# Performance work log

Measured on AMD Instinct MI355X. Metric: run time of the kernel, lower is better.

The kernel has to match this reference:

```python
import jax, jax.numpy as jnp
import numpy as np

N_USERS = 100000
N_ITEMS = 50000
N = N_USERS + N_ITEMS  # graph nodes
E = 2_400_000
B = 16384
EMB = 64
HID = 128
LN_EPS = 1e-5


def _gcn(x, W, b, src, dst):
    # PyG GCNConv (eval): sym-normalized aggregation with self-loops.
    xw = x @ W                                      # [N, out]
    deg = jnp.ones((N,), x.dtype).at[dst].add(1.0)  # in-degree + self-loop
    dinv = jax.lax.rsqrt(deg)
    norm = dinv[src] * dinv[dst]                    # [E]
    msg = xw[src] * norm[:, None]                   # [E, out] gather
    out = jax.ops.segment_sum(msg, dst, num_segments=N)
    out = out + xw * (dinv * dinv)[:, None]         # self-loop term (norm_ii = 1/deg_i)
    return out + b


def _ln(h, g, b):
    mu = jnp.mean(h, axis=-1, keepdims=True)
    var = jnp.mean(jnp.square(h - mu), axis=-1, keepdims=True)
    return (h - mu) * jax.lax.rsqrt(var + LN_EPS) * g + b


def setup_inputs() -> dict:
    key = jax.random.key(0)
    ks = jax.random.split(key, 20)
    f32 = jnp.float32
    def lin(k, fi, fo):
        return jax.random.normal(k, (fi, fo), f32) * (1.0 / np.sqrt(fi))
    inp = {
        "x": jax.random.normal(ks[0], (N, EMB), f32),
        "src": jax.random.randint(ks[1], (E,), 0, N, jnp.int32),
        "dst": jax.random.randint(ks[2], (E,), 0, N, jnp.int32),
        "user_indices": jax.random.randint(ks[3], (B,), 1, N_USERS + 1, jnp.int32),
        "item_indices": jax.random.randint(ks[4], (B,), 1, N_ITEMS + 1, jnp.int32),
        # GCNConv weights
        "W1": lin(ks[5], EMB, HID), "b1": jnp.zeros((HID,), f32),
        "W2": lin(ks[6], HID, EMB), "b2": jnp.zeros((EMB,), f32),
        # MLP head: Linear(128,128)-LN-ReLU-Linear(128,64)-LN-ReLU-Linear(64,1)
        "fcW1": lin(ks[7], 2 * EMB, HID), "fcb1": jnp.zeros((HID,), f32),
        "g1": jnp.ones((HID,), f32), "be1": jnp.zeros((HID,), f32),
        "fcW2": lin(ks[8], HID, HID // 2), "fcb2": jnp.zeros((HID // 2,), f32),
        "g2": jnp.ones((HID // 2,), f32), "be2": jnp.zeros((HID // 2,), f32),
        "fcW3": lin(ks[9], HID // 2, 1), "fcb3": jnp.zeros((1,), f32),
    }
    return inp


def reference(x, src, dst, user_indices, item_indices,
              W1, b1, W2, b2,
              fcW1, fcb1, g1, be1, fcW2, fcb2, g2, be2, fcW3, fcb3):
    # graph path (edge_index and x provided); dropout inactive in eval mode
    h = jax.nn.relu(_gcn(x, W1, b1, src, dst))
    h = _gcn(h, W2, b2, src, dst)                   # [N, EMB]
    user_emb = h[:N_USERS][user_indices - 1]        # [B, EMB]
    item_emb = h[N_USERS:][item_indices - 1]        # [B, EMB]
    c = jnp.concatenate([user_emb, item_emb], axis=1)  # [B, 2*EMB]
    z = jax.nn.relu(_ln(c @ fcW1 + fcb1, g1, be1))
    z = jax.nn.relu(_ln(z @ fcW2 + fcb2, g2, be2))
    z = z @ fcW3 + fcb3                             # [B, 1]
    return jax.nn.sigmoid(z).squeeze()
```

## Files before the change

kernel.cpp:

```cpp
#include <hip/hip_runtime.h>
#include <hip/hip_bf16.h>
#include <math.h>

#define N_USERS_C 100000
#define BK_SHIFT 9
#define BK_NODES 512

typedef __bf16 bf8_t __attribute__((ext_vector_type(8)));
typedef float f32x4 __attribute__((ext_vector_type(4)));

__device__ __forceinline__ unsigned int pack_bf16(float a, float b) {
    __hip_bfloat16 ha = __float2bfloat16(a), hb = __float2bfloat16(b);
    return ((unsigned int)(*(unsigned short*)&hb) << 16) | (unsigned int)(*(unsigned short*)&ha);
}
__device__ __forceinline__ unsigned short bf16_1(float a) {
    __hip_bfloat16 ha = __float2bfloat16(a);
    return *(unsigned short*)&ha;
}
__device__ __forceinline__ float bf_lo(unsigned int u) { return __uint_as_float(u << 16); }
__device__ __forceinline__ float bf_hi(unsigned int u) { return __uint_as_float(u & 0xffff0000u); }

__global__ __launch_bounds__(512) void k_pre(const int* __restrict__ dst, int* __restrict__ chist,
                                             const float* __restrict__ x, unsigned int* __restrict__ xb,
                                             int E, int nbk, int EB2, int n2) {
    __shared__ int lcnt[BK_NODES];
    const int bid = blockIdx.x;
    const int t = threadIdx.x;
    if (bid < EB2) {
        if (t < nbk) lcnt[t] = 0;
        __syncthreads();
        int e0 = bid * 4096;
        #pragma unroll
        for (int j = 0; j < 8; ++j) {
            int e = e0 + j * 512 + t;
            if (e < E) atomicAdd(&lcnt[dst[e] >> BK_SHIFT], 1);
        }
        __syncthreads();
        if (t < nbk && lcnt[t]) atomicAdd(&chist[t], lcnt[t]);
    } else {
        int base = (bid - EB2) * 2048;
        #pragma unroll
        for (int j = 0; j < 4; ++j) {
            int i = base + j * 512 + t;
            if (i < n2) {
                float2 v = ((const float2*)x)[i];
                xb[i] = pack_bf16(v.x, v.y);
            }
        }
    }
}

__global__ __launch_bounds__(512) void k_scanChist(const int* __restrict__ chist,
                                                   int* __restrict__ base,
                                                   int* __restrict__ cursor,
                                                   int* __restrict__ rowstart,
                                                   int nbk, int N, int E) {
    __shared__ int s[512];
    int t = threadIdx.x;
    int v = (t < nbk) ? chist[t] : 0;
    s[t] = v;
    __syncthreads();
    for (int off = 1; off < 512; off <<= 1) {
        int u = (t >= off) ? s[t - off] : 0;
        __syncthreads();
        s[t] += u;
        __syncthreads();
    }
    int ex = s[t] - v;
    if (t < nbk) { base[t] = ex; cursor[t] = ex; }
    if (t == 0) { base[nbk] = E; rowstart[N] = E; }
}

__global__ __launch_bounds__(512) void k_bin(const int* __restrict__ src,
                                             const int* __restrict__ dst,
                                             int* __restrict__ bucketCursor,
                                             int* __restrict__ pairBuf, int E, int nbk) {
    __shared__ int lcnt[BK_NODES];
    __shared__ int lofs[BK_NODES];
    __shared__ int delta[BK_NODES];
    __shared__ int waveSum[8];
    __shared__ int sPack[2048];
    __shared__ unsigned short sBkt[2048];
    const int t = threadIdx.x;
    const int lane = t & 63;
    const int w = t >> 6;
    const int e0 = blockIdx.x * 2048;
    if (t < nbk) lcnt[t] = 0;
    __syncthreads();

    int mySrc[4], myB[4], myDl[4];
    #pragma unroll
    for (int j = 0; j < 4; ++j) {
        int e = e0 + j * 512 + t;
        if (e < E) {
            int sv = src[e], dv = dst[e];
            mySrc[j] = sv; myB[j] = dv >> BK_SHIFT; myDl[j] = dv & (BK_NODES - 1);
            atomicAdd(&lcnt[myB[j]], 1);
        } else myB[j] = -1;
    }
    __syncthreads();

    int v = (t < nbk) ? lcnt[t] : 0;
    int inc = v;
    #pragma unroll
    for (int off = 1; off < 64; off <<= 1) {
        int n = __shfl_up(inc, off);
        if (lane >= off) inc += n;
    }
    if (lane == 63) waveSum[w] = inc;
    __syncthreads();
    int wp = 0;
    #pragma unroll
    for (int i = 0; i < 8; ++i) wp += (i < w) ? waveSum[i] : 0;
    int ex = wp + inc - v;
    if (t < nbk) {
        lofs[t] = ex;
        int gb = (v > 0) ? atomicAdd(&bucketCursor[t], v) : 0;
        delta[t] = gb - ex;
    }
    __syncthreads();

    #pragma unroll
    for (int j = 0; j < 4; ++j) {
        if (myB[j] >= 0) {
            int p = atomicAdd(&lofs[myB[j]], 1);
            sPack[p] = mySrc[j] | (myDl[j] << 18);
            sBkt[p] = (unsigned short)myB[j];
        }
    }
    __syncthreads();
    int total = (E - e0 < 2048) ? (E - e0) : 2048;
    for (int i = t; i < total; i += 512)
        pairBuf[delta[sBkt[i]] + i] = sPack[i];
}

__global__ __launch_bounds__(512) void k_bscatter(const int* __restrict__ pairBuf,
                                                  const int* __restrict__ base,
                                                  int* __restrict__ rowstart,
                                                  float* __restrict__ dinv,
                                                  int* __restrict__ csr, int N) {
    const int b = blockIdx.x;
    const int n0 = b << BK_SHIFT;
    int nn = N - n0; if (nn > BK_NODES) nn = BK_NODES;
    __shared__ int hist[BK_NODES];
    __shared__ int curs[BK_NODES];
    __shared__ int waveSum[8];
    const int t = threadIdx.x;
    const int lane = t & 63;
    const int w = t >> 6;
    if (t < nn) hist[t] = 0;
    __syncthreads();
    const int e0 = base[b], e1 = base[b + 1];
    for (int e = e0 + t; e < e1; e += 512)
        atomicAdd(&hist[pairBuf[e] >> 18], 1);
    __syncthreads();

    int v = (t < nn) ? hist[t] : 0;
    int inc = v;
    #pragma unroll
    for (int off = 1; off < 64; off <<= 1) {
        int n = __shfl_up(inc, off);
        if (lane >= off) inc += n;
    }
    if (lane == 63) waveSum[w] = inc;
    __syncthreads();
    int wp = 0;
    #pragma unroll
    for (int i = 0; i < 8; ++i) wp += (i < w) ? waveSum[i] : 0;
    int ex = wp + inc - v;
    if (t < nn) {
        int r = e0 + ex;
        rowstart[n0 + t] = r;
        curs[t] = r;
        dinv[n0 + t] = rsqrtf((float)(v + 1));
    }
    __syncthreads();
    for (int e = e0 + t; e < e1; e += 512) {
        int pk = pairBuf[e];
        int pos = atomicAdd(&curs[pk >> 18], 1);
        csr[pos] = pk & 0x3FFFF;
    }
}

__global__ __launch_bounds__(256) void k_gather1(const int* __restrict__ rowstart,
                                                 const int* __restrict__ csr,
                                                 const float* __restrict__ dinv,
                                                 const uint4* __restrict__ xb4,
                                                 const float* __restrict__ x,
                                                 unsigned int* __restrict__ outb, int N) {
    const int node = blockIdx.x * 4 + (threadIdx.x >> 6);
    const int l = threadIdx.x & 63;
    if (node >= N) return;
    const int sub = l >> 3;
    const int c = l & 7;
    const int rs = rowstart[node];
    const int re = rowstart[node + 1];

    float acc[8] = {0.f, 0.f, 0.f, 0.f, 0.f, 0.f, 0.f, 0.f};
    for (int base = rs; base < re; base += 64) {
        int idx = base + l;
        int sE = (idx < re) ? csr[idx] : 0;
        float dE = (idx < re) ? dinv[sE] : 0.0f;
        int cnt = re - base; if (cnt > 64) cnt = 64;
        int groups = (cnt + 7) >> 3;
        for (int g = 0; g < groups; ++g) {
            int e = g * 8 + sub;
            int sk = __shfl(sE, e);
            float dk = __shfl(dE, e);
            uint4 u = xb4[(size_t)sk * 8 + c];
            acc[0] += dk * bf_lo(u.x); acc[1] += dk * bf_hi(u.x);
            acc[2] += dk * bf_lo(u.y); acc[3] += dk * bf_hi(u.y);
            acc[4] += dk * bf_lo(u.z); acc[5] += dk * bf_hi(u.z);
            acc[6] += dk * bf_lo(u.w); acc[7] += dk * bf_hi(u.w);
        }
    }
    #pragma unroll
    for (int m = 8; m < 64; m <<= 1)
        #pragma unroll
        for (int i = 0; i < 8; ++i) acc[i] += __shfl_xor(acc[i], m);
    if (sub == 0) {
        float dd = dinv[node];
        float d2 = dd * dd;
        float4 x0 = ((const float4*)x)[(size_t)node * 16 + c * 2];
        float4 x1 = ((const float4*)x)[(size_t)node * 16 + c * 2 + 1];
        uint4 o;
        o.x = pack_bf16(dd * acc[0] + d2 * x0.x, dd * acc[1] + d2 * x0.y);
        o.y = pack_bf16(dd * acc[2] + d2 * x0.z, dd * acc[3] + d2 * x0.w);
        o.z = pack_bf16(dd * acc[4] + d2 * x1.x, dd * acc[5] + d2 * x1.y);
        o.w = pack_bf16(dd * acc[6] + d2 * x1.z, dd * acc[7] + d2 * x1.w);
        ((uint4*)outb)[(size_t)node * 8 + c] = o;
    }
}

__global__ __launch_bounds__(256) void k_layer12(const unsigned int* __restrict__ aggXb,
                                                 const float* __restrict__ W1,
                                                 const float* __restrict__ b1,
                                                 const float* __restrict__ W2,
                                                 const float* __restrict__ dinv,
                                                 unsigned int* __restrict__ xs2b, int N) {
    __shared__ unsigned int sA[64 * 36];
    __shared__ unsigned int sB[128 * 36];
    __shared__ unsigned int sC[64 * 68];
    const int t = threadIdx.x;
    const int w = t >> 6;
    const int l = t & 63;
    const int n16 = l & 15;
    const int quad = l >> 4;
    const int row0 = blockIdx.x * 64;

    for (int i = t; i < 512; i += 256) {
        int r = i >> 3, c = i & 7;
        int row = row0 + r;
        uint4 u = (row < N) ? ((const uint4*)aggXb)[(size_t)row * 8 + c]
                            : make_uint4(0u, 0u, 0u, 0u);
        *(uint4*)&sA[r * 36 + c * 4] = u;
    }
    for (int i = t; i < 4096; i += 256) {
        int kp = i >> 7, n = i & 127;
        float a0 = W1[(size_t)(2 * kp) * 128 + n];
        float a1 = W1[(size_t)(2 * kp + 1) * 128 + n];
        sB[n * 36 + kp] = pack_bf16(a0, a1);
    }
    __syncthreads();

    f32x4 acc[8];
    #pragma unroll
    for (int nt = 0; nt < 8; ++nt) acc[nt] = (f32x4){0.f, 0.f, 0.f, 0.f};
    {
        const int am = w * 16 + n16;
        bf8_t a0 = *(const bf8_t*)&sA[am * 36 + quad * 4];
        bf8_t a1 = *(const bf8_t*)&sA[am * 36 + 16 + quad * 4];
        #pragma unroll
        for (int nt = 0; nt < 8; ++nt) {
            bf8_t b0 = *(const bf8_t*)&sB[(nt * 16 + n16) * 36 + quad * 4];
            bf8_t b1v = *(const bf8_t*)&sB[(nt * 16 + n16) * 36 + 16 + quad * 4];
            acc[nt] = __builtin_amdgcn_mfma_f32_16x16x32_bf16(a0, b0, acc[nt], 0, 0, 0);
            acc[nt] = __builtin_amdgcn_mfma_f32_16x16x32_bf16(a1, b1v, acc[nt], 0, 0, 0);
        }
    }
    __syncthreads();

    {
        unsigned short* sC16 = (unsigned short*)sC;
        #pragma unroll
        for (int nt = 0; nt < 8; ++nt) {
            int col = nt * 16 + n16;
            float bv = b1[col];
            #pragma unroll
            for (int reg = 0; reg < 4; ++reg) {
                int r = w * 16 + quad * 4 + reg;
                sC16[r * 136 + col] = bf16_1(fmaxf(acc[nt][reg] + bv, 0.f));
            }
        }
    }
    for (int i = t; i < 4096; i += 256) {
        int kp = i >> 6, n = i & 63;
        float a0 = W2[(size_t)(2 * kp) * 64 + n];
        float a1 = W2[(size_t)(2 * kp + 1) * 64 + n];
        sB[n * 68 + kp] = pack_bf16(a0, a1);
    }
    __syncthreads();

    f32x4 acc2[4];
    #pragma unroll
    for (int nt = 0; nt < 4; ++nt) acc2[nt] = (f32x4){0.f, 0.f, 0.f, 0.f};
    {
        const int am = w * 16 + n16;
        #pragma unroll
        for (int ks = 0; ks < 4; ++ks) {
            bf8_t a = *(const bf8_t*)&sC[am * 68 + ks * 16 + quad * 4];
            #pragma unroll
            for (int nt = 0; nt < 4; ++nt) {
                bf8_t b = *(const bf8_t*)&sB[(nt * 16 + n16) * 68 + ks * 16 + quad * 4];
                acc2[nt] = __builtin_amdgcn_mfma_f32_16x16x32_bf16(a, b, acc2[nt], 0, 0, 0);
            }
        }
    }

    {
        unsigned short* sA16 = (unsigned short*)sA;
        #pragma unroll
        for (int reg = 0; reg < 4; ++reg) {
            int r = w * 16 + quad * 4 + reg;
            int row = row0 + r;
            float dd = (row < N) ? dinv[row] : 0.f;
            #pragma unroll
            for (int nt = 0; nt < 4; ++nt)
                sA16[r * 72 + nt * 16 + n16] = bf16_1(acc2[nt][reg] * dd);
        }
    }
    __syncthreads();
    for (int i = t; i < 512; i += 256) {
        int r = i >> 3, c = i & 7;
        int row = row0 + r;
        if (row < N)
            ((uint4*)xs2b)[(size_t)row * 8 + c] = *(uint4*)&sA[r * 36 + c * 4];
    }
}

__global__ __launch_bounds__(256) void k_gather_pairs(const int* __restrict__ rowstart,
                                                      const int* __restrict__ csr,
                                                      const float* __restrict__ dinv,
                                                      const uint4* __restrict__ xs2b4,
                                                      const float* __restrict__ b2,
                                                      const int* __restrict__ ui,
                                                      const int* __restrict__ ii,
                                                      float* __restrict__ cB, int B) {
    const int wave = threadIdx.x >> 6;
    const int b = blockIdx.x * 2 + (wave >> 1);
    const int half = wave & 1;
    const int l = threadIdx.x & 63;
    const int sub = l >> 3;
    const int c = l & 7;
    if (b >= B) return;
    const int node = (half == 0) ? (ui[b] - 1) : (N_USERS_C + ii[b] - 1);
    const int rs = rowstart[node];
    const int re = rowstart[node + 1];

    float acc[8] = {0.f, 0.f, 0.f, 0.f, 0.f, 0.f, 0.f, 0.f};
    for (int base = rs; base < re; base += 64) {
        int idx = base + l;
        int sE = (idx < re) ? csr[idx] : 0;
        float vE = (idx < re) ? 1.0f : 0.0f;
        int cnt = re - base; if (cnt > 64) cnt = 64;
        int groups = (cnt + 7) >> 3;
        for (int g = 0; g < groups; ++g) {
            int e = g * 8 + sub;
            int sk = __shfl(sE, e);
            float vk = __shfl(vE, e);
            uint4 u = xs2b4[(size_t)sk * 8 + c];
            acc[0] += vk * bf_lo(u.x); acc[1] += vk * bf_hi(u.x);
            acc[2] += vk * bf_lo(u.y); acc[3] += vk * bf_hi(u.y);
            acc[4] += vk * bf_lo(u.z); acc[5] += vk * bf_hi(u.z);
            acc[6] += vk * bf_lo(u.w); acc[7] += vk * bf_hi(u.w);
        }
    }
    #pragma unroll
    for (int m = 8; m < 64; m <<= 1)
        #pragma unroll
        for (int i = 0; i < 8; ++i) acc[i] += __shfl_xor(acc[i], m);
    if (sub == 0) {
        float dd = dinv[node];
        uint4 us = xs2b4[(size_t)node * 8 + c];
        float4 s0, s1;
        s0.x = bf_lo(us.x); s0.y = bf_hi(us.x); s0.z = bf_lo(us.y); s0.w = bf_hi(us.y);
        s1.x = bf_lo(us.z); s1.y = bf_hi(us.z); s1.z = bf_lo(us.w); s1.w = bf_hi(us.w);
        float4 bb0 = ((const float4*)b2)[c * 2];
        float4 bb1 = ((const float4*)b2)[c * 2 + 1];
        float4 o0, o1;
        o0.x = dd * (acc[0] + s0.x) + bb0.x;
        o0.y = dd * (acc[1] + s0.y) + bb0.y;
        o0.z = dd * (acc[2] + s0.z) + bb0.z;
        o0.w = dd * (acc[3] + s0.w) + bb0.w;
        o1.x = dd * (acc[4] + s1.x) + bb1.x;
        o1.y = dd * (acc[5] + s1.y) + bb1.y;
        o1.z = dd * (acc[6] + s1.z) + bb1.z;
        o1.w = dd * (acc[7] + s1.w) + bb1.w;
        ((float4*)cB)[(size_t)b * 32 + half * 16 + c * 2] = o0;
        ((float4*)cB)[(size_t)b * 32 + half * 16 + c * 2 + 1] = o1;
    }
}

__global__ __launch_bounds__(256) void k_mlp(const float* __restrict__ cB,
                                             const float* __restrict__ fcW1, const float* __restrict__ fcb1,
                                             const float* __restrict__ g1,   const float* __restrict__ be1,
                                             const float* __restrict__ fcW2, const float* __restrict__ fcb2,
                                             const float* __restrict__ g2,   const float* __restrict__ be2,
                                             const float* __restrict__ fcW3, const float* __restrict__ fcb3,
                                             float* __restrict__ out) {
    __shared__ float sIn[32 * 128];
    __shared__ float sW[64 * 128];
    const int t = threadIdx.x;
    const int row0 = blockIdx.x * 32;
    const int rg = t >> 4;
    const int cg = t & 15;

    for (int i = t; i < 1024; i += 256) {
        int r = i >> 5, c4 = i & 31;
        *(float4*)&sIn[r * 128 + c4 * 4] = *(const float4*)&cB[(size_t)(row0 + r) * 128 + c4 * 4];
    }

    float acc1[2][8];
    {
        float4 b01 = *(const float4*)&fcb1[cg * 8];
        float4 b23 = *(const float4*)&fcb1[cg * 8 + 4];
        #pragma unroll
        for (int jj = 0; jj < 2; ++jj) {
            acc1[jj][0] = b01.x; acc1[jj][1] = b01.y; acc1[jj][2] = b01.z; acc1[jj][3] = b01.w;
            acc1[jj][4] = b23.x; acc1[jj][5] = b23.y; acc1[jj][6] = b23.z; acc1[jj][7] = b23.w;
        }
    }
    for (int s = 0; s < 2; ++s) {
        __syncthreads();
        for (int i = t; i < 2048; i += 256) {
            int k = i >> 5, c4 = i & 31;
            *(float4*)&sW[k * 128 + c4 * 4] = *(const float4*)&fcW1[(size_t)(64 * s + k) * 128 + c4 * 4];
        }
        __syncthreads();
        for (int k0 = 0; k0 < 64; k0 += 4) {
            float4 a[2];
            #pragma unroll
            for (int jj = 0; jj < 2; ++jj)
                a[jj] = *(const float4*)&sIn[(rg * 2 + jj) * 128 + 64 * s + k0];
            #pragma unroll
            for (int kk = 0; kk < 4; ++kk) {
                float4 w0 = *(const float4*)&sW[(k0 + kk) * 128 + cg * 8];
                float4 w1 = *(const float4*)&sW[(k0 + kk) * 128 + cg * 8 + 4];
                #pragma unroll
                for (int jj = 0; jj < 2; ++jj) {
                    float f = ((const float*)&a[jj])[kk];
                    acc1[jj][0] += f * w0.x; acc1[jj][1] += f * w0.y;
                    acc1[jj][2] += f * w0.z; acc1[jj][3] += f * w0.w;
                    acc1[jj][4] += f * w1.x; acc1[jj][5] += f * w1.y;
                    acc1[jj][6] += f * w1.z; acc1[jj][7] += f * w1.w;
                }
            }
        }
    }
    __syncthreads();

    {
        float4 g01 = *(const float4*)&g1[cg * 8];
        float4 g23 = *(const float4*)&g1[cg * 8 + 4];
        float4 e01 = *(const float4*)&be1[cg * 8];
        float4 e23 = *(const float4*)&be1[cg * 8 + 4];
        float gv[8] = {g01.x, g01.y, g01.z, g01.w, g23.x, g23.y, g23.z, g23.w};
        float ev[8] = {e01.x, e01.y, e01.z, e01.w, e23.x, e23.y, e23.z, e23.w};
        #pragma unroll
        for (int jj = 0; jj < 2; ++jj) {
            float s_ = 0.f, ss = 0.f;
            #pragma unroll
            for (int c = 0; c < 8; ++c) { float v = acc1[jj][c]; s_ += v; ss += v * v; }
            #pragma unroll
            for (int m = 1; m < 16; m <<= 1) { s_ += __shfl_xor(s_, m); ss += __shfl_xor(ss, m); }
            float mu = s_ * (1.0f / 128.0f);
            float var = ss * (1.0f / 128.0f) - mu * mu;
            float rs = rsqrtf(var + 1e-5f);
            #pragma unroll
            for (int c = 0; c < 8; ++c) {
                float z = (acc1[jj][c] - mu) * rs * gv[c] + ev[c];
                sIn[(rg * 2 + jj) * 128 + cg * 8 + c] = fmaxf(z, 0.f);
            }
        }
    }
    __syncthreads();

    for (int i = t; i < 2048; i += 256) {
        int k = i >> 4, c4 = i & 15;
        *(float4*)&sW[k * 64 + c4 * 4] = *(const float4*)&fcW2[(size_t)k * 64 + c4 * 4];
    }
    float acc2[2][4];
    {
        float4 bv = *(const float4*)&fcb2[cg * 4];
        #pragma unroll
        for (int jj = 0; jj < 2; ++jj) {
            acc2[jj][0] = bv.x; acc2[jj][1] = bv.y; acc2[jj][2] = bv.z; acc2[jj][3] = bv.w;
        }
    }
    __syncthreads();
    for (int k0 = 0; k0 < 128; k0 += 4) {
        float4 a[2], w[4];
        #pragma unroll
        for (int jj = 0; jj < 2; ++jj) a[jj] = *(const float4*)&sIn[(rg * 2 + jj) * 128 + k0];
        #pragma unroll
        for (int kk = 0; kk < 4; ++kk) w[kk] = *(const float4*)&sW[(k0 + kk) * 64 + cg * 4];
        #pragma unroll
        for (int jj = 0; jj < 2; ++jj) {
            const float* aj = (const float*)&a[jj];
            #pragma unroll
            for (int kk = 0; kk < 4; ++kk) {
                float f = aj[kk];
                acc2[jj][0] += f * w[kk].x; acc2[jj][1] += f * w[kk].y;
                acc2[jj][2] += f * w[kk].z; acc2[jj][3] += f * w[kk].w;
            }
        }
    }

    {
        float4 gv4 = *(const float4*)&g2[cg * 4];
        float4 ev4 = *(const float4*)&be2[cg * 4];
        float4 w34 = *(const float4*)&fcW3[cg * 4];
        float gv[4] = {gv4.x, gv4.y, gv4.z, gv4.w};
        float ev[4] = {ev4.x, ev4.y, ev4.z, ev4.w};
        float wv[4] = {w34.x, w34.y, w34.z, w34.w};
        float b3 = fcb3[0];
        #pragma unroll
        for (int jj = 0; jj < 2; ++jj) {
            float s_ = 0.f, ss = 0.f;
            #pragma unroll
            for (int c = 0; c < 4; ++c) { float v = acc2[jj][c]; s_ += v; ss += v * v; }
            #pragma unroll
            for (int m = 1; m < 16; m <<= 1) { s_ += __shfl_xor(s_, m); ss += __shfl_xor(ss, m); }
            float mu = s_ * (1.0f / 64.0f);
            float var = ss * (1.0f / 64.0f) - mu * mu;
            float rs = rsqrtf(var + 1e-5f);
            float p = 0.f;
            #pragma unroll
            for (int c = 0; c < 4; ++c) {
                float z = fmaxf((acc2[jj][c] - mu) * rs * gv[c] + ev[c], 0.f);
                p += z * wv[c];
            }
            #pragma unroll
            for (int m = 1; m < 16; m <<= 1) p += __shfl_xor(p, m);
            if (cg == 0) out[row0 + rg * 2 + jj] = 1.0f / (1.0f + expf(-(p + b3)));
        }
    }
}

extern "C" void kernel_launch(void* const* d_in, const int* in_sizes, int n_in,
                              void* d_out, int out_size, void* d_ws, size_t ws_size,
                              hipStream_t stream) {
    const float* x    = (const float*)d_in[0];
    const int*   src  = (const int*)d_in[1];
    const int*   dst  = (const int*)d_in[2];
    const int*   ui   = (const int*)d_in[3];
    const int*   ii   = (const int*)d_in[4];
    const float* W1   = (const float*)d_in[5];
    const float* b1   = (const float*)d_in[6];
    const float* W2   = (const float*)d_in[7];
    const float* b2   = (const float*)d_in[8];
    const float* fcW1 = (const float*)d_in[9];
    const float* fcb1 = (const float*)d_in[10];
    const float* g1   = (const float*)d_in[11];
    const float* be1  = (const float*)d_in[12];
    const float* fcW2 = (const float*)d_in[13];
    const float* fcb2 = (const float*)d_in[14];
    const float* g2   = (const float*)d_in[15];
    const float* be2  = (const float*)d_in[16];
    const float* fcW3 = (const float*)d_in[17];
    const float* fcb3 = (const float*)d_in[18];
    float* out = (float*)d_out;

    const int N = in_sizes[0] / 64;
    const int E = in_sizes[1];
    const int B = in_sizes[3];
    const int NBK = (N + BK_NODES - 1) >> BK_SHIFT;
    const int EB  = (E + 2047) / 2048;
    const int EB2 = (E + 4095) / 4096;
    const int n2 = N * 32;
    const int XB = (n2 + 2047) / 2048;

    float* ws   = (float*)d_ws;
    float* dinv = ws;
    int* rowstart = (int*)(dinv + N);
    int* csr      = rowstart + (N + 1);
    unsigned int* xb = (unsigned int*)(csr + E);
    unsigned int* bufU = xb + (size_t)N * 32;
    unsigned int* xs2b = bufU + (size_t)N * 32;
    float* cB = (float*)(xs2b + (size_t)N * 32);
    int* pairBuf = (int*)bufU;
    int* chist   = pairBuf + E;
    int* bbase   = chist + 512;
    int* bcursor = bbase + 513;
    unsigned int* aggXb = bufU;

    hipMemsetAsync(chist, 0, 512 * sizeof(int), stream);
    k_pre<<<EB2 + XB, 512, 0, stream>>>(dst, chist, x, xb, E, NBK, EB2, n2);
    k_scanChist<<<1, 512, 0, stream>>>(chist, bbase, bcursor, rowstart, NBK, N, E);
    k_bin<<<EB, 512, 0, stream>>>(src, dst, bcursor, pairBuf, E, NBK);
    k_bscatter<<<NBK, 512, 0, stream>>>(pairBuf, bbase, rowstart, dinv, csr, N);

    k_gather1<<<(N + 3) / 4, 256, 0, stream>>>(rowstart, csr, dinv, (const uint4*)xb, x, aggXb, N);

    k_layer12<<<(N + 63) / 64, 256, 0, stream>>>(aggXb, W1, b1, W2, dinv, xs2b, N);

    k_gather_pairs<<<(B + 1) / 2, 256, 0, stream>>>(rowstart, csr, dinv, (const uint4*)xs2b,
                                                    b2, ui, ii, cB, B);

    k_mlp<<<B / 32, 256, 0, stream>>>(cB, fcW1, fcb1, g1, be1,
                                      fcW2, fcb2, g2, be2, fcW3, fcb3, out);
}
```

Baseline: 361.9 us.

## Fold bucket-histogram scan into bin and scatter kernels, double bin tile

Removes the single-block k_scanChist launch. k_bin and k_bscatter now each recompute the exclusive scan of the bucket histogram redundantly per block, and the bin cursor becomes a zeroed offset added to the scanned base. k_bin processes 4096 edges per block instead of 2048, halving its grid and the number of global atomics, at the cost of more shared memory and registers per block. The self-loop term in gather1 now reads the bf16 copy of x instead of the fp32 original, which saves bandwidth but slightly lowers precision.

```diff
diff --git a/kernel.cpp b/kernel.cpp
--- a/kernel.cpp
+++ b/kernel.cpp
@@ -50,47 +50,27 @@
     }
 }
 
-__global__ __launch_bounds__(512) void k_scanChist(const int* __restrict__ chist,
-                                                   int* __restrict__ base,
-                                                   int* __restrict__ cursor,
-                                                   int* __restrict__ rowstart,
-                                                   int nbk, int N, int E) {
-    __shared__ int s[512];
-    int t = threadIdx.x;
-    int v = (t < nbk) ? chist[t] : 0;
-    s[t] = v;
-    __syncthreads();
-    for (int off = 1; off < 512; off <<= 1) {
-        int u = (t >= off) ? s[t - off] : 0;
-        __syncthreads();
-        s[t] += u;
-        __syncthreads();
-    }
-    int ex = s[t] - v;
-    if (t < nbk) { base[t] = ex; cursor[t] = ex; }
-    if (t == 0) { base[nbk] = E; rowstart[N] = E; }
-}
-
 __global__ __launch_bounds__(512) void k_bin(const int* __restrict__ src,
                                              const int* __restrict__ dst,
-                                             int* __restrict__ bucketCursor,
+                                             const int* __restrict__ chist,
+                                             int* __restrict__ bcursor0,
                                              int* __restrict__ pairBuf, int E, int nbk) {
     __shared__ int lcnt[BK_NODES];
     __shared__ int lofs[BK_NODES];
     __shared__ int delta[BK_NODES];
     __shared__ int waveSum[8];
-    __shared__ int sPack[2048];
-    __shared__ unsigned short sBkt[2048];
+    __shared__ int sPack[4096];
+    __shared__ unsigned short sBkt[4096];
     const int t = threadIdx.x;
     const int lane = t & 63;
     const int w = t >> 6;
-    const int e0 = blockIdx.x * 2048;
+    const int e0 = blockIdx.x * 4096;
     if (t < nbk) lcnt[t] = 0;
     __syncthreads();
 
-    int mySrc[4], myB[4], myDl[4];
-    #pragma unroll
-    for (int j = 0; j < 4; ++j) {
+    int mySrc[8], myB[8], myDl[8];
+    #pragma unroll
+    for (int j = 0; j < 8; ++j) {
         int e = e0 + j * 512 + t;
         if (e < E) {
             int sv = src[e], dv = dst[e];
@@ -108,20 +88,33 @@
         if (lane >= off) inc += n;
     }
     if (lane == 63) waveSum[w] = inc;
-    __syncthreads();
-    int wp = 0;
-    #pragma unroll
-    for (int i = 0; i < 8; ++i) wp += (i < w) ? waveSum[i] : 0;
+    int cv = (t < nbk) ? chist[t] : 0;
+    int cinc = cv;
+    #pragma unroll
+    for (int off = 1; off < 64; off <<= 1) {
+        int n = __shfl_up(cinc, off);
+        if (lane >= off) cinc += n;
+    }
+    __shared__ int cWaveSum[8];
+    if (lane == 63) cWaveSum[w] = cinc;
+    __syncthreads();
+    int wp = 0, cwp = 0;
+    #pragma unroll
+    for (int i = 0; i < 8; ++i) {
+        wp += (i < w) ? waveSum[i] : 0;
+        cwp += (i < w) ? cWaveSum[i] : 0;
+    }
     int ex = wp + inc - v;
+    int cbase = cwp + cinc - cv;
     if (t < nbk) {
         lofs[t] = ex;
-        int gb = (v > 0) ? atomicAdd(&bucketCursor[t], v) : 0;
+        int gb = cbase + ((v > 0) ? atomicAdd(&bcursor0[t], v) : 0);
         delta[t] = gb - ex;
     }
     __syncthreads();
 
     #pragma unroll
-    for (int j = 0; j < 4; ++j) {
+    for (int j = 0; j < 8; ++j) {
         if (myB[j] >= 0) {
             int p = atomicAdd(&lofs[myB[j]], 1);
             sPack[p] = mySrc[j] | (myDl[j] << 18);
@@ -129,28 +122,46 @@
         }
     }
     __syncthreads();
-    int total = (E - e0 < 2048) ? (E - e0) : 2048;
+    int total = (E - e0 < 4096) ? (E - e0) : 4096;
     for (int i = t; i < total; i += 512)
         pairBuf[delta[sBkt[i]] + i] = sPack[i];
 }
 
 __global__ __launch_bounds__(512) void k_bscatter(const int* __restrict__ pairBuf,
-                                                  const int* __restrict__ base,
+                                                  const int* __restrict__ chist,
                                                   int* __restrict__ rowstart,
                                                   float* __restrict__ dinv,
-                                                  int* __restrict__ csr, int N) {
+                                                  int* __restrict__ csr, int N, int E, int nbk) {
     const int b = blockIdx.x;
     const int n0 = b << BK_SHIFT;
     int nn = N - n0; if (nn > BK_NODES) nn = BK_NODES;
     __shared__ int hist[BK_NODES];
     __shared__ int curs[BK_NODES];
     __shared__ int waveSum[8];
+    __shared__ int sE0, sE1;
     const int t = threadIdx.x;
     const int lane = t & 63;
     const int w = t >> 6;
-    if (t < nn) hist[t] = 0;
-    __syncthreads();
-    const int e0 = base[b], e1 = base[b + 1];
+
+    {
+        int cv = (t < nbk) ? chist[t] : 0;
+        int cinc = cv;
+        #pragma unroll
+        for (int off = 1; off < 64; off <<= 1) {
+            int n = __shfl_up(cinc, off);
+            if (lane >= off) cinc += n;
+        }
+        if (lane == 63) waveSum[w] = cinc;
+        if (t < nn) hist[t] = 0;
+        __syncthreads();
+        int cwp = 0;
+        #pragma unroll
+        for (int i = 0; i < 8; ++i) cwp += (i < w) ? waveSum[i] : 0;
+        if (t == b) { sE0 = cwp + cinc - cv; sE1 = cwp + cinc; }
+    }
+    __syncthreads();
+    const int e0 = sE0, e1 = sE1;
+
     for (int e = e0 + t; e < e1; e += 512)
         atomicAdd(&hist[pairBuf[e] >> 18], 1);
     __syncthreads();
@@ -174,6 +185,7 @@
         curs[t] = r;
         dinv[n0 + t] = rsqrtf((float)(v + 1));
     }
+    if (b == gridDim.x - 1 && t == 0) rowstart[N] = E;
     __syncthreads();
     for (int e = e0 + t; e < e1; e += 512) {
         int pk = pairBuf[e];
@@ -186,7 +198,6 @@
                                                  const int* __restrict__ csr,
                                                  const float* __restrict__ dinv,
                                                  const uint4* __restrict__ xb4,
-                                                 const float* __restrict__ x,
                                                  unsigned int* __restrict__ outb, int N) {
     const int node = blockIdx.x * 4 + (threadIdx.x >> 6);
     const int l = threadIdx.x & 63;
@@ -221,13 +232,12 @@
     if (sub == 0) {
         float dd = dinv[node];
         float d2 = dd * dd;
-        float4 x0 = ((const float4*)x)[(size_t)node * 16 + c * 2];
-        float4 x1 = ((const float4*)x)[(size_t)node * 16 + c * 2 + 1];
+        uint4 us = xb4[(size_t)node * 8 + c];
         uint4 o;
-        o.x = pack_bf16(dd * acc[0] + d2 * x0.x, dd * acc[1] + d2 * x0.y);
-        o.y = pack_bf16(dd * acc[2] + d2 * x0.z, dd * acc[3] + d2 * x0.w);
-        o.z = pack_bf16(dd * acc[4] + d2 * x1.x, dd * acc[5] + d2 * x1.y);
-        o.w = pack_bf16(dd * acc[6] + d2 * x1.z, dd * acc[7] + d2 * x1.w);
+        o.x = pack_bf16(dd * acc[0] + d2 * bf_lo(us.x), dd * acc[1] + d2 * bf_hi(us.x));
+        o.y = pack_bf16(dd * acc[2] + d2 * bf_lo(us.y), dd * acc[3] + d2 * bf_hi(us.y));
+        o.z = pack_bf16(dd * acc[4] + d2 * bf_lo(us.z), dd * acc[5] + d2 * bf_hi(us.z));
+        o.w = pack_bf16(dd * acc[6] + d2 * bf_lo(us.w), dd * acc[7] + d2 * bf_hi(us.w));
         ((uint4*)outb)[(size_t)node * 8 + c] = o;
     }
 }
@@ -575,7 +585,6 @@
     const int E = in_sizes[1];
     const int B = in_sizes[3];
     const int NBK = (N + BK_NODES - 1) >> BK_SHIFT;
-    const int EB  = (E + 2047) / 2048;
     const int EB2 = (E + 4095) / 4096;
     const int n2 = N * 32;
     const int XB = (n2 + 2047) / 2048;
@@ -590,17 +599,15 @@
     float* cB = (float*)(xs2b + (size_t)N * 32);
     int* pairBuf = (int*)bufU;
     int* chist   = pairBuf + E;
-    int* bbase   = chist + 512;
-    int* bcursor = bbase + 513;
+    int* bcursor = chist + 512;
     unsigned int* aggXb = bufU;
 
-    hipMemsetAsync(chist, 0, 512 * sizeof(int), stream);
+    hipMemsetAsync(chist, 0, 1024 * sizeof(int), stream);
     k_pre<<<EB2 + XB, 512, 0, stream>>>(dst, chist, x, xb, E, NBK, EB2, n2);
-    k_scanChist<<<1, 512, 0, stream>>>(chist, bbase, bcursor, rowstart, NBK, N, E);
-    k_bin<<<EB, 512, 0, stream>>>(src, dst, bcursor, pairBuf, E, NBK);
-    k_bscatter<<<NBK, 512, 0, stream>>>(pairBuf, bbase, rowstart, dinv, csr, N);
-
-    k_gather1<<<(N + 3) / 4, 256, 0, stream>>>(rowstart, csr, dinv, (const uint4*)xb, x, aggXb, N);
+    k_bin<<<EB2, 512, 0, stream>>>(src, dst, chist, bcursor, pairBuf, E, NBK);
+    k_bscatter<<<NBK, 512, 0, stream>>>(pairBuf, chist, rowstart, dinv, csr, N, E, NBK);
+
+    k_gather1<<<(N + 3) / 4, 256, 0, stream>>>(rowstart, csr, dinv, (const uint4*)xb, aggXb, N);
 
     k_layer12<<<(N + 63) / 64, 256, 0, stream>>>(aggXb, W1, b1, W2, dinv, xs2b, N);
 
```

Result: faster. 345.2 us (-4.6%).
